# Optimization experiments

Hardware: AMD Instinct MI355X
Metric: run time of the kernel (lower is better)

Reference implementation:

```python
import jax, jax.numpy as jnp
import numpy as np

DIM = 2048
NUM_HEADS = 16
HEAD_DIM = DIM // NUM_HEADS  # 128
LATENT = 512
THETA = 10000.0


def rotate_half(x):
    # interleaved rotate: (x0,x1,x2,x3,...) -> (-x1,x0,-x3,x2,...)
    x1 = x[..., ::2]
    x2 = x[..., 1::2]
    return jnp.stack((-x2, x1), axis=-1).reshape(x.shape)


def apply_rope(x, sin, cos):
    return x * cos + rotate_half(x) * sin


def setup_inputs() -> dict:
    key = jax.random.key(0)
    ks = jax.random.split(key, 6)
    s_in = 1.0 / np.sqrt(DIM)
    s_lat = 1.0 / np.sqrt(LATENT)
    x = jax.random.normal(ks[0], (2, 2048, DIM), dtype=jnp.float32)
    Wq = jax.random.normal(ks[1], (DIM, DIM), dtype=jnp.float32) * s_in
    Wdkv = jax.random.normal(ks[2], (DIM, 2 * LATENT), dtype=jnp.float32) * s_in
    Wuk = jax.random.normal(ks[3], (LATENT, DIM), dtype=jnp.float32) * s_lat
    Wuv = jax.random.normal(ks[4], (LATENT, DIM), dtype=jnp.float32) * s_lat
    Wo = jax.random.normal(ks[5], (DIM, DIM), dtype=jnp.float32) * s_in
    return {"x": x, "Wq": Wq, "Wdkv": Wdkv, "Wuk": Wuk, "Wuv": Wuv, "Wo": Wo}


def reference(x, Wq, Wdkv, Wuk, Wuv, Wo):
    b, s, _ = x.shape
    # q projection -> [b, h, s, hd]
    q = (x @ Wq).reshape(b, s, NUM_HEADS, HEAD_DIM).transpose(0, 2, 1, 3)
    # low-rank latent down-projection, then up-project K and V
    dkv = x @ Wdkv  # [b, s, 2*L]
    dk, dv = dkv[..., :LATENT], dkv[..., LATENT:]
    k = (dk @ Wuk).reshape(b, s, NUM_HEADS, HEAD_DIM).transpose(0, 2, 1, 3)
    v = (dv @ Wuv).reshape(b, s, NUM_HEADS, HEAD_DIM).transpose(0, 2, 1, 3)
    # RoPE cache (concatenated freqs, matching the torch module)
    inv_freq = 1.0 / (THETA ** (jnp.arange(0, HEAD_DIM, 2, dtype=jnp.float32) / HEAD_DIM))
    t = jnp.arange(s, dtype=jnp.float32)
    freqs = t[:, None] * inv_freq[None, :]          # [s, hd/2]
    emb = jnp.concatenate([freqs, freqs], axis=-1)  # [s, hd]
    sin, cos = jnp.sin(emb), jnp.cos(emb)
    q = apply_rope(q, sin, cos)
    k = apply_rope(k, sin, cos)
    # SDPA (no mask, no dropout): scale = 1/sqrt(head_dim)
    scores = jnp.einsum('bhqd,bhkd->bhqk', q, k) / jnp.sqrt(jnp.float32(HEAD_DIM))
    attn = jax.nn.softmax(scores, axis=-1)
    out = jnp.einsum('bhqk,bhkd->bhqd', attn, v)
    out = out.transpose(0, 2, 1, 3).reshape(b, s, DIM)
    return out @ Wo
```

## Files before the change

### kernel.cpp

```cpp
#include <hip/hip_runtime.h>
#include <hip/hip_bf16.h>
#include <stdint.h>

typedef __attribute__((ext_vector_type(8))) __bf16 bf16x8;
typedef __attribute__((ext_vector_type(4))) float f32x4;

__device__ __forceinline__ unsigned short f2bf(float f) {
  union { float f; unsigned u; } v; v.f = f;
  unsigned r = v.u + 0x7FFFu + ((v.u >> 16) & 1u);
  return (unsigned short)(r >> 16);
}

__device__ __forceinline__ float fast_exp2(float x) {
#if __has_builtin(__builtin_amdgcn_exp2f)
  return __builtin_amdgcn_exp2f(x);
#else
  return exp2f(x);
#endif
}

__device__ __forceinline__ void gload_lds16(const void* g, void* l) {
  __builtin_amdgcn_global_load_lds((const __attribute__((address_space(1))) void*)g,
                                   (__attribute__((address_space(3))) void*)l,
                                   16, 0, 0);
}


__global__ void k_rope(float* __restrict__ cosT, float* __restrict__ sinT) {
  int idx = blockIdx.x * blockDim.x + threadIdx.x;
  int t = idx >> 6, j = idx & 63;
  float inv = powf(10000.f, -(float)j / 64.f);
  float ang = (float)t * inv;
  cosT[idx] = cosf(ang);
  sinT[idx] = sinf(ang);
}

__global__ void k_cvt_bf16(const float* __restrict__ in, unsigned short* __restrict__ out, int n) {
  int i = (blockIdx.x * blockDim.x + threadIdx.x) * 4;
  if (i >= n) return;
  float4 v = *reinterpret_cast<const float4*>(in + i);
  ushort4 o;
  o.x = f2bf(v.x); o.y = f2bf(v.y); o.z = f2bf(v.z); o.w = f2bf(v.w);
  *reinterpret_cast<ushort4*>(out + i) = o;
}

__global__ __launch_bounds__(256) void k_transpose_cvt(const float* __restrict__ in,
                                                       unsigned short* __restrict__ out,
                                                       int K, int N) {
  __shared__ float t[32][33];
  int nt = blockIdx.x, kt = blockIdx.y;
  int tx = threadIdx.x, ty = threadIdx.y;
#pragma unroll
  for (int i = 0; i < 4; i++)
    t[ty + i * 8][tx] = in[(size_t)(kt * 32 + ty + i * 8) * N + nt * 32 + tx];
  __syncthreads();
#pragma unroll
  for (int i = 0; i < 4; i++)
    out[(size_t)(nt * 32 + ty + i * 8) * K + kt * 32 + tx] = f2bf(t[tx][ty + i * 8]);
}

template <int EPI>
__global__ __launch_bounds__(256, 2) void k_gemm(
    const unsigned short* __restrict__ A, int lda,
    const unsigned short* __restrict__ BT, int ldb,
    void* __restrict__ Cout, int M, int N, int K,
    const float* __restrict__ cosT, const float* __restrict__ sinT) {
  __shared__ __attribute__((aligned(16))) unsigned short As[128 * 64];
  __shared__ __attribute__((aligned(16))) unsigned short Bs[128 * 64];
  const int tid = threadIdx.x;
  const int lane = tid & 63;
  const int w = tid >> 6;
  const int wr = w >> 1, wc = w & 1;
  const int m0 = blockIdx.y * 128, n0 = blockIdx.x * 128;

  f32x4 acc[4][4] = {};

  const int srow = w * 8 + (lane >> 3);
  const int sch = (lane & 7) * 8;
  const unsigned short* gA = A + (size_t)(m0 + srow) * lda + sch;
  const unsigned short* gB = BT + (size_t)(n0 + srow) * ldb + sch;
  unsigned short* lA = &As[srow * 64 + sch];
  unsigned short* lB = &Bs[srow * 64 + sch];

  for (int kt = 0; kt < K; kt += 64) {
    __syncthreads();
#pragma unroll
    for (int i = 0; i < 4; i++) {
      gload_lds16(gA + (size_t)(i * 32) * lda + kt, lA + i * 32 * 64);
      gload_lds16(gB + (size_t)(i * 32) * ldb + kt, lB + i * 32 * 64);
    }
    __syncthreads();
#pragma unroll
    for (int kk = 0; kk < 64; kk += 32) {
      bf16x8 af[4], bfr[4];
#pragma unroll
      for (int m = 0; m < 4; m++)
        af[m] = *reinterpret_cast<const bf16x8*>(&As[(wr * 64 + m * 16 + (lane & 15)) * 64 + kk + (lane >> 4) * 8]);
#pragma unroll
      for (int n = 0; n < 4; n++)
        bfr[n] = *reinterpret_cast<const bf16x8*>(&Bs[(wc * 64 + n * 16 + (lane & 15)) * 64 + kk + (lane >> 4) * 8]);
#pragma unroll
      for (int m = 0; m < 4; m++)
#pragma unroll
        for (int n = 0; n < 4; n++) {
          if (EPI == 3)
            acc[m][n] = __builtin_amdgcn_mfma_f32_16x16x32_bf16(bfr[n], af[m], acc[m][n], 0, 0, 0);
          else
            acc[m][n] = __builtin_amdgcn_mfma_f32_16x16x32_bf16(af[m], bfr[n], acc[m][n], 0, 0, 0);
        }
    }
  }

  const int rl = (lane >> 4) * 4;
  const int cl = lane & 15;
#pragma unroll
  for (int m = 0; m < 4; m++)
#pragma unroll
    for (int n = 0; n < 4; n++)
#pragma unroll
      for (int r = 0; r < 4; r++) {
        float v = acc[m][n][r];
        if (EPI == 0) {
          int gr = m0 + wr * 64 + m * 16 + rl + r;
          int gc = n0 + wc * 64 + n * 16 + cl;
          ((unsigned short*)Cout)[(size_t)gr * N + gc] = f2bf(v);
        } else if (EPI == 4) {
          int gr = m0 + wr * 64 + m * 16 + rl + r;
          int gc = n0 + wc * 64 + n * 16 + cl;
          ((float*)Cout)[(size_t)gr * N + gc] = v;
        } else if (EPI == 1 || EPI == 2) {
          int gr = m0 + wr * 64 + m * 16 + rl + r;
          int gc = n0 + wc * 64 + n * 16 + cl;
          int b = gr >> 11, s = gr & 2047, h = gc >> 7, d = gc & 127;
          if (EPI == 1) {
            float p = __shfl_xor(v, 1);
            float c = cosT[s * 64 + (d & 63)];
            float sn = sinT[s * 64 + (d & 63)];
            v = v * c + ((d & 1) ? p : -p) * sn;
          }
          ((unsigned short*)Cout)[((size_t)(b * 16 + h) * 2048 + s) * 128 + d] = f2bf(v);
        } else {
          int gd = n0 + wc * 64 + n * 16 + rl + r;
          int gs = m0 + wr * 64 + m * 16 + cl;
          int b = gs >> 11, s = gs & 2047, h = gd >> 7, d = gd & 127;
          ((unsigned short*)Cout)[((size_t)(b * 16 + h) * 128 + d) * 2048 + s] = f2bf(v);
        }
      }
}

__global__ __launch_bounds__(256, 2) void k_attn(
    const unsigned short* __restrict__ Q,
    const unsigned short* __restrict__ Kt,
    const unsigned short* __restrict__ Vt,
    unsigned short* __restrict__ O) {
  __shared__ __attribute__((aligned(16))) unsigned short Kls[2][64 * 128];
  __shared__ __attribute__((aligned(16))) unsigned short Vls[2][128 * 64];
  __shared__ __attribute__((aligned(16))) unsigned short Pls[128 * 64];
  const int qt = blockIdx.x, bh = blockIdx.y;
  const int tid = threadIdx.x, lane = tid & 63, w = tid >> 6;
  const unsigned short* Qh = Q + (size_t)bh * 2048 * 128;
  const unsigned short* Kh = Kt + (size_t)bh * 2048 * 128;
  const unsigned short* Vh = Vt + (size_t)bh * 128 * 2048;
  const int q0 = qt * 128;

  bf16x8 qf[2][4];
#pragma unroll
  for (int m = 0; m < 2; m++)
#pragma unroll
    for (int kd = 0; kd < 4; kd++) {
      int row = q0 + w * 32 + m * 16 + (lane & 15);
      int k = kd * 32 + (lane >> 4) * 8;
      qf[m][kd] = *reinterpret_cast<const bf16x8*>(Qh + (size_t)row * 128 + k);
    }

  f32x4 accO[2][8] = {};
  float lsum[2][4] = {};

  const int kr0 = w * 4 + (lane >> 4);
  const int kcb = lane & 15;
  const int vr0 = w * 8 + (lane >> 3);
  const int vcb = lane & 7;

  auto stage = [&](int buf, int kt) {
#pragma unroll
    for (int i = 0; i < 4; i++) {
      int rr = kr0 + i * 16;
      gload_lds16(Kh + (size_t)(kt * 64 + rr) * 128 + ((kcb ^ (rr & 7)) * 8),
                  (char*)Kls + buf * 16384 + rr * 256 + kcb * 16);
    }
#pragma unroll
    for (int i = 0; i < 4; i++) {
      int rr = vr0 + i * 32;
      gload_lds16(Vh + (size_t)rr * 2048 + kt * 64 + ((vcb ^ (rr & 7)) * 8),
                  (char*)Vls + buf * 16384 + rr * 128 + vcb * 16);
    }
  };

  stage(0, 0);
  __syncthreads();

  const float CL2 = 0.08838834764831845f * 1.44269504088896f;

  for (int kt = 0; kt < 32; kt++) {
    const int cur = kt & 1;
    if (kt + 1 < 32) stage(cur ^ 1, kt + 1);

    f32x4 accS[2][4] = {};
#pragma unroll
    for (int kd = 0; kd < 4; kd++) {
      bf16x8 kf[4];
#pragma unroll
      for (int n = 0; n < 4; n++) {
        int row = n * 16 + (lane & 15);
        int byte = cur * 16384 + row * 256 + (((kd * 32 + (lane >> 4) * 8) * 2) ^ ((row & 7) << 4));
        kf[n] = *reinterpret_cast<const bf16x8*>((const char*)Kls + byte);
      }
#pragma unroll
      for (int m = 0; m < 2; m++)
#pragma unroll
        for (int n = 0; n < 4; n++)
          accS[m][n] = __builtin_amdgcn_mfma_f32_16x16x32_bf16(qf[m][kd], kf[n], accS[m][n], 0, 0, 0);
    }

#pragma unroll
    for (int m = 0; m < 2; m++)
#pragma unroll
      for (int n = 0; n < 4; n++)
#pragma unroll
        for (int r = 0; r < 4; r++) {
          float p = fast_exp2(accS[m][n][r] * CL2);
          lsum[m][r] += p;
          int row = w * 32 + m * 16 + (lane >> 4) * 4 + r;
          int byte = row * 128 + (((n * 16 + (lane & 15)) * 2) ^ ((row & 7) << 4));
          *(unsigned short*)((char*)Pls + byte) = f2bf(p);
        }

#pragma unroll
    for (int kk = 0; kk < 2; kk++) {
      bf16x8 pf[2], vf[8];
#pragma unroll
      for (int m = 0; m < 2; m++) {
        int row = w * 32 + m * 16 + (lane & 15);
        int byte = row * 128 + (((kk * 32 + (lane >> 4) * 8) * 2) ^ ((row & 7) << 4));
        pf[m] = *reinterpret_cast<const bf16x8*>((const char*)Pls + byte);
      }
#pragma unroll
      for (int n = 0; n < 8; n++) {
        int row = n * 16 + (lane & 15);
        int byte = cur * 16384 + row * 128 + (((kk * 32 + (lane >> 4) * 8) * 2) ^ ((row & 7) << 4));
        vf[n] = *reinterpret_cast<const bf16x8*>((const char*)Vls + byte);
      }
#pragma unroll
      for (int m = 0; m < 2; m++)
#pragma unroll
        for (int n = 0; n < 8; n++)
          accO[m][n] = __builtin_amdgcn_mfma_f32_16x16x32_bf16(pf[m], vf[n], accO[m][n], 0, 0, 0);
    }

    __syncthreads();
  }

  float rinv[2][4];
#pragma unroll
  for (int m = 0; m < 2; m++)
#pragma unroll
    for (int r = 0; r < 4; r++) {
      float s = lsum[m][r];
      s += __shfl_xor(s, 1);
      s += __shfl_xor(s, 2);
      s += __shfl_xor(s, 4);
      s += __shfl_xor(s, 8);
      rinv[m][r] = 1.0f / s;
    }

  const int b = bh >> 4, h = bh & 15;
#pragma unroll
  for (int m = 0; m < 2; m++)
#pragma unroll
    for (int n = 0; n < 8; n++)
#pragma unroll
      for (int r = 0; r < 4; r++) {
        int s = q0 + w * 32 + m * 16 + (lane >> 4) * 4 + r;
        int d = n * 16 + (lane & 15);
        O[((size_t)(b * 2048 + s)) * 2048 + h * 128 + d] = f2bf(accO[m][n][r] * rinv[m][r]);
      }
}


extern "C" void kernel_launch(void* const* d_in, const int* in_sizes, int n_in,
                              void* d_out, int out_size, void* d_ws, size_t ws_size,
                              hipStream_t stream) {
  const float* x    = (const float*)d_in[0];
  const float* Wq   = (const float*)d_in[1];
  const float* Wdkv = (const float*)d_in[2];
  const float* Wuk  = (const float*)d_in[3];
  const float* Wuv  = (const float*)d_in[4];
  const float* Wo   = (const float*)d_in[5];

  char* ws = (char*)d_ws;
  unsigned short* xb    = (unsigned short*)(ws + 0);
  unsigned short* WqT   = (unsigned short*)(ws + 16777216);
  unsigned short* WdkvT = (unsigned short*)(ws + 25165824);
  unsigned short* WukT  = (unsigned short*)(ws + 29360128);
  unsigned short* WuvT  = (unsigned short*)(ws + 31457280);
  unsigned short* dkv   = (unsigned short*)(ws + 33554432);
  unsigned short* q_att = (unsigned short*)(ws + 41943040);
  unsigned short* k_att = (unsigned short*)(ws + 58720256);
  unsigned short* vT    = (unsigned short*)(ws + 75497472);
  float* cosT           = (float*)(ws + 92274688);
  float* sinT           = (float*)(ws + 92798976);

  k_rope<<<512, 256, 0, stream>>>(cosT, sinT);
  k_cvt_bf16<<<8192, 256, 0, stream>>>(x, xb, 2 * 2048 * 2048);
  k_transpose_cvt<<<dim3(64, 64), dim3(32, 8), 0, stream>>>(Wq, WqT, 2048, 2048);
  k_transpose_cvt<<<dim3(32, 64), dim3(32, 8), 0, stream>>>(Wdkv, WdkvT, 2048, 1024);
  k_transpose_cvt<<<dim3(64, 16), dim3(32, 8), 0, stream>>>(Wuk, WukT, 512, 2048);
  k_transpose_cvt<<<dim3(64, 16), dim3(32, 8), 0, stream>>>(Wuv, WuvT, 512, 2048);

  k_gemm<1><<<dim3(16, 32), 256, 0, stream>>>(xb, 2048, WqT, 2048, q_att, 4096, 2048, 2048, cosT, sinT);
  k_gemm<0><<<dim3(8, 32), 256, 0, stream>>>(xb, 2048, WdkvT, 2048, dkv, 4096, 1024, 2048, nullptr, nullptr);
  k_transpose_cvt<<<dim3(64, 64), dim3(32, 8), 0, stream>>>(Wo, WqT, 2048, 2048);
  k_gemm<1><<<dim3(16, 32), 256, 0, stream>>>(dkv, 1024, WukT, 512, k_att, 4096, 2048, 512, cosT, sinT);
  k_gemm<3><<<dim3(16, 32), 256, 0, stream>>>(dkv + 512, 1024, WuvT, 512, vT, 4096, 2048, 512, nullptr, nullptr);
  k_attn<<<dim3(16, 32), 256, 0, stream>>>(q_att, k_att, vT, xb);
  k_gemm<4><<<dim3(16, 32), 256, 0, stream>>>(xb, 2048, WqT, 2048, (float*)d_out, 4096, 2048, 2048, nullptr, nullptr);
}
```

Before: 292.4 us.

## Double-buffer GEMM LDS tiles and fuse Q and KV-down projections

The GEMM kernel now keeps two LDS buffers for A and B. It issues the global-to-LDS loads for the next K tile before computing on the current one, with one barrier per iteration instead of two, so load latency can overlap MFMA work. The Q projection and the latent down-projection are merged into one launch over N=3072, since WqT and WdkvT sit next to each other in the workspace. A new epilogue sends columns below 2048 to the RoPE/head-major Q output and the rest to dkv. The cost is double the LDS per block (64KB), which could limit occupancy, and a branch inside the epilogue.

```diff
diff --git a/kernel.cpp b/kernel.cpp
--- a/kernel.cpp
+++ b/kernel.cpp
@@ -63,10 +63,10 @@
 __global__ __launch_bounds__(256, 2) void k_gemm(
     const unsigned short* __restrict__ A, int lda,
     const unsigned short* __restrict__ BT, int ldb,
-    void* __restrict__ Cout, int M, int N, int K,
+    void* __restrict__ Cout, void* __restrict__ Cout2, int M, int N, int K,
     const float* __restrict__ cosT, const float* __restrict__ sinT) {
-  __shared__ __attribute__((aligned(16))) unsigned short As[128 * 64];
-  __shared__ __attribute__((aligned(16))) unsigned short Bs[128 * 64];
+  __shared__ __attribute__((aligned(16))) unsigned short As[2][128 * 64];
+  __shared__ __attribute__((aligned(16))) unsigned short Bs[2][128 * 64];
   const int tid = threadIdx.x;
   const int lane = tid & 63;
   const int w = tid >> 6;
@@ -79,26 +79,31 @@
   const int sch = (lane & 7) * 8;
   const unsigned short* gA = A + (size_t)(m0 + srow) * lda + sch;
   const unsigned short* gB = BT + (size_t)(n0 + srow) * ldb + sch;
-  unsigned short* lA = &As[srow * 64 + sch];
-  unsigned short* lB = &Bs[srow * 64 + sch];
-
-  for (int kt = 0; kt < K; kt += 64) {
-    __syncthreads();
+
+  auto stage = [&](int buf, int kofs) {
 #pragma unroll
     for (int i = 0; i < 4; i++) {
-      gload_lds16(gA + (size_t)(i * 32) * lda + kt, lA + i * 32 * 64);
-      gload_lds16(gB + (size_t)(i * 32) * ldb + kt, lB + i * 32 * 64);
-    }
-    __syncthreads();
+      gload_lds16(gA + (size_t)(i * 32) * lda + kofs, &As[buf][(srow + i * 32) * 64 + sch]);
+      gload_lds16(gB + (size_t)(i * 32) * ldb + kofs, &Bs[buf][(srow + i * 32) * 64 + sch]);
+    }
+  };
+
+  stage(0, 0);
+  __syncthreads();
+
+  const int nk = K >> 6;
+  for (int kt = 0; kt < nk; kt++) {
+    const int cur = kt & 1;
+    if (kt + 1 < nk) stage(cur ^ 1, (kt + 1) << 6);
 #pragma unroll
     for (int kk = 0; kk < 64; kk += 32) {
       bf16x8 af[4], bfr[4];
 #pragma unroll
       for (int m = 0; m < 4; m++)
-        af[m] = *reinterpret_cast<const bf16x8*>(&As[(wr * 64 + m * 16 + (lane & 15)) * 64 + kk + (lane >> 4) * 8]);
+        af[m] = *reinterpret_cast<const bf16x8*>(&As[cur][(wr * 64 + m * 16 + (lane & 15)) * 64 + kk + (lane >> 4) * 8]);
 #pragma unroll
       for (int n = 0; n < 4; n++)
-        bfr[n] = *reinterpret_cast<const bf16x8*>(&Bs[(wc * 64 + n * 16 + (lane & 15)) * 64 + kk + (lane >> 4) * 8]);
+        bfr[n] = *reinterpret_cast<const bf16x8*>(&Bs[cur][(wc * 64 + n * 16 + (lane & 15)) * 64 + kk + (lane >> 4) * 8]);
 #pragma unroll
       for (int m = 0; m < 4; m++)
 #pragma unroll
@@ -109,6 +114,7 @@
             acc[m][n] = __builtin_amdgcn_mfma_f32_16x16x32_bf16(af[m], bfr[n], acc[m][n], 0, 0, 0);
         }
     }
+    __syncthreads();
   }
 
   const int rl = (lane >> 4) * 4;
@@ -120,25 +126,32 @@
 #pragma unroll
       for (int r = 0; r < 4; r++) {
         float v = acc[m][n][r];
-        if (EPI == 0) {
-          int gr = m0 + wr * 64 + m * 16 + rl + r;
-          int gc = n0 + wc * 64 + n * 16 + cl;
-          ((unsigned short*)Cout)[(size_t)gr * N + gc] = f2bf(v);
-        } else if (EPI == 4) {
+        if (EPI == 4) {
           int gr = m0 + wr * 64 + m * 16 + rl + r;
           int gc = n0 + wc * 64 + n * 16 + cl;
           ((float*)Cout)[(size_t)gr * N + gc] = v;
-        } else if (EPI == 1 || EPI == 2) {
+        } else if (EPI == 1) {
           int gr = m0 + wr * 64 + m * 16 + rl + r;
           int gc = n0 + wc * 64 + n * 16 + cl;
           int b = gr >> 11, s = gr & 2047, h = gc >> 7, d = gc & 127;
-          if (EPI == 1) {
+          float p = __shfl_xor(v, 1);
+          float c = cosT[s * 64 + (d & 63)];
+          float sn = sinT[s * 64 + (d & 63)];
+          v = v * c + ((d & 1) ? p : -p) * sn;
+          ((unsigned short*)Cout)[((size_t)(b * 16 + h) * 2048 + s) * 128 + d] = f2bf(v);
+        } else if (EPI == 5) {
+          int gr = m0 + wr * 64 + m * 16 + rl + r;
+          int gc = n0 + wc * 64 + n * 16 + cl;
+          if (n0 < 2048) {
+            int b = gr >> 11, s = gr & 2047, h = gc >> 7, d = gc & 127;
             float p = __shfl_xor(v, 1);
             float c = cosT[s * 64 + (d & 63)];
             float sn = sinT[s * 64 + (d & 63)];
             v = v * c + ((d & 1) ? p : -p) * sn;
+            ((unsigned short*)Cout)[((size_t)(b * 16 + h) * 2048 + s) * 128 + d] = f2bf(v);
+          } else {
+            ((unsigned short*)Cout2)[(size_t)gr * 1024 + (gc - 2048)] = f2bf(v);
           }
-          ((unsigned short*)Cout)[((size_t)(b * 16 + h) * 2048 + s) * 128 + d] = f2bf(v);
         } else {
           int gd = n0 + wc * 64 + n * 16 + rl + r;
           int gs = m0 + wr * 64 + m * 16 + cl;
@@ -317,11 +330,10 @@
   k_transpose_cvt<<<dim3(64, 16), dim3(32, 8), 0, stream>>>(Wuk, WukT, 512, 2048);
   k_transpose_cvt<<<dim3(64, 16), dim3(32, 8), 0, stream>>>(Wuv, WuvT, 512, 2048);
 
-  k_gemm<1><<<dim3(16, 32), 256, 0, stream>>>(xb, 2048, WqT, 2048, q_att, 4096, 2048, 2048, cosT, sinT);
-  k_gemm<0><<<dim3(8, 32), 256, 0, stream>>>(xb, 2048, WdkvT, 2048, dkv, 4096, 1024, 2048, nullptr, nullptr);
+  k_gemm<5><<<dim3(24, 32), 256, 0, stream>>>(xb, 2048, WqT, 2048, q_att, dkv, 4096, 3072, 2048, cosT, sinT);
   k_transpose_cvt<<<dim3(64, 64), dim3(32, 8), 0, stream>>>(Wo, WqT, 2048, 2048);
-  k_gemm<1><<<dim3(16, 32), 256, 0, stream>>>(dkv, 1024, WukT, 512, k_att, 4096, 2048, 512, cosT, sinT);
-  k_gemm<3><<<dim3(16, 32), 256, 0, stream>>>(dkv + 512, 1024, WuvT, 512, vT, 4096, 2048, 512, nullptr, nullptr);
+  k_gemm<1><<<dim3(16, 32), 256, 0, stream>>>(dkv, 1024, WukT, 512, k_att, nullptr, 4096, 2048, 512, cosT, sinT);
+  k_gemm<3><<<dim3(16, 32), 256, 0, stream>>>(dkv + 512, 1024, WuvT, 512, vT, nullptr, 4096, 2048, 512, nullptr, nullptr);
   k_attn<<<dim3(16, 32), 256, 0, stream>>>(q_att, k_att, vT, xb);
-  k_gemm<4><<<dim3(16, 32), 256, 0, stream>>>(xb, 2048, WqT, 2048, (float*)d_out, 4096, 2048, 2048, nullptr, nullptr);
-}
+  k_gemm<4><<<dim3(16, 32), 256, 0, stream>>>(xb, 2048, WqT, 2048, (float*)d_out, nullptr, 4096, 2048, 2048, nullptr, nullptr);
+}
```

New measurement: 315.7 us. +8.0%, slower.
